# Kernel optimization log

Measured on AMD Instinct MI355X. Metric: run time of the kernel, lower is better.

## Reference

```python
import jax, jax.numpy as jnp
import numpy as np
import math

RATIOS = [2, 4, 8, 16]   # attn_aggr_ratio per path
HEAD_DIM = 64
EPS = 1e-5               # BatchNorm1d eps (eval mode, running stats)


def _bn(x, g, b, m, v):
    # x: (N, C, L); per-channel eval-mode BatchNorm1d
    inv = g / jnp.sqrt(v + EPS)
    return x * inv[None, :, None] + (b - m * inv)[None, :, None]


def _conv1(x, W, b=None):
    # 1x1 Conv1d == channel matmul. x: (N, Cin, L), W: (Cout, Cin)
    y = jnp.einsum('ncl,dc->ndl', x, W)
    if b is not None:
        y = y + b[None, :, None]
    return y


def setup_inputs() -> dict:
    key = jax.random.key(0)
    ks = iter(jax.random.split(key, 16))
    N, C, L = 8, 512, 3072
    P, d = 4, C // 4
    FF = 4 * C
    w = lambda shape: jax.random.normal(next(ks), shape, dtype=jnp.float32) * 0.05
    inp = {'x': jax.random.normal(next(ks), (N, C, L), dtype=jnp.float32)}
    for nm in ('norm1', 'norm2'):
        inp[nm + '_g'] = jnp.ones((C,), jnp.float32)
        inp[nm + '_b'] = jnp.zeros((C,), jnp.float32)
        inp[nm + '_m'] = jnp.zeros((C,), jnp.float32)
        inp[nm + '_v'] = jnp.ones((C,), jnp.float32)
    for nm in ('Wq', 'Wk', 'Wv', 'Wo', 'Wp'):
        inp[nm] = w((P, d, d))
    for nm in ('bq', 'bk', 'bv', 'bo'):
        inp[nm] = jnp.zeros((P, d), jnp.float32)
    for nm in ('ag', 'an'):  # aggr-block BN and pre-KV BN, per path
        inp[nm + '_g'] = jnp.ones((P, d), jnp.float32)
        inp[nm + '_b'] = jnp.zeros((P, d), jnp.float32)
        inp[nm + '_m'] = jnp.zeros((P, d), jnp.float32)
        inp[nm + '_v'] = jnp.ones((P, d), jnp.float32)
    inp['W1'] = w((FF, C)); inp['b1'] = jnp.zeros((FF,), jnp.float32)
    inp['W2'] = w((C, FF)); inp['b2'] = jnp.zeros((C,), jnp.float32)
    return inp


def reference(x, norm1_g, norm1_b, norm1_m, norm1_v,
              Wq, bq, Wk, bk, Wv, bv, Wo, bo, Wp,
              ag_g, ag_b, ag_m, ag_v, an_g, an_b, an_m, an_v,
              norm2_g, norm2_b, norm2_m, norm2_v,
              W1, b1, W2, b2):
    N, C, L = x.shape
    P = len(RATIOS)
    d = C // P
    h = _bn(x, norm1_g, norm1_b, norm1_m, norm1_v)
    outs = []
    for i, r in enumerate(RATIOS):  # small fixed set of paths
        xi = h[:, i * d:(i + 1) * d, :]                       # (N, d, L)
        q = _conv1(xi, Wq[i], bq[i])                          # (N, d, L)
        # local aware aggregation: avg_pool + max_pool (L divisible by r)
        xp = xi.reshape(N, d, L // r, r)
        xa = xp.mean(-1) + xp.max(-1)                         # (N, d, L/r)
        xa = _bn(_conv1(xa, Wp[i]), ag_g[i], ag_b[i], ag_m[i], ag_v[i])
        xa = _bn(xa, an_g[i], an_b[i], an_m[i], an_v[i])
        k = _conv1(xa, Wk[i], bk[i])
        v = _conv1(xa, Wv[i], bv[i])
        Nh = d // HEAD_DIM
        Lk = L // r
        qh = q.reshape(N, Nh, HEAD_DIM, L) / math.sqrt(HEAD_DIM)
        kh = k.reshape(N, Nh, HEAD_DIM, Lk)
        vh = v.reshape(N, Nh, HEAD_DIM, Lk)
        attn = jax.nn.softmax(jnp.einsum('nhel,nhem->nhlm', qh, kh), axis=-1)
        o = jnp.einsum('nhlm,nhem->nhel', attn, vh).reshape(N, d, L)
        outs.append(_conv1(o, Wo[i], bo[i]))
    x = x + jnp.concatenate(outs, axis=1)                     # residual
    h2 = _bn(x, norm2_g, norm2_b, norm2_m, norm2_v)
    m = jax.nn.gelu(_conv1(h2, W1, b1))
    m = _conv1(m, W2, b2)
    return x + m
```

## Files before the change

kernel.cpp:

```cpp
#include <hip/hip_runtime.h>
#include <math.h>

#define EPS 1e-5f

#define F_BIAS  1
#define F_DBN   2
#define F_GELU  4
#define F_RESID 8

typedef __attribute__((ext_vector_type(8))) __bf16 bf16x8;
typedef __attribute__((ext_vector_type(4))) float f32x4;
typedef __attribute__((ext_vector_type(8))) unsigned short u16x8;

__device__ __forceinline__ unsigned int pack2bf(float a, float b) {
    unsigned short ua = __builtin_bit_cast(unsigned short, (__bf16)a);
    unsigned short ub = __builtin_bit_cast(unsigned short, (__bf16)b);
    return (unsigned int)ua | ((unsigned int)ub << 16);
}

__device__ __forceinline__ void gload_lds16(const unsigned short* g, unsigned short* l) {
    __builtin_amdgcn_global_load_lds(
        (const __attribute__((address_space(1))) unsigned int*)g,
        (__attribute__((address_space(3))) unsigned int*)l,
        16, 0, 0);
}

__device__ __forceinline__ float gelu_f(float u) {
    float s = u * u;
    float w = u * fmaf(s, 0.0713548162726f, 1.59576912161f);
    float e = __expf(-w);
    return u * __builtin_amdgcn_rcpf(1.f + e);
}

__device__ __constant__ int c_LKS[4]  = {1536, 768, 384, 192};
__device__ __constant__ int c_OFFB[4] = {0, 1572864, 2359296, 2752512};

__global__ __launch_bounds__(256) void wcvt_kernel(
    const float* __restrict__ Wq, const float* __restrict__ Wk,
    const float* __restrict__ Wv, const float* __restrict__ Wo,
    const float* __restrict__ Wp, const float* __restrict__ W1,
    const float* __restrict__ W2, unsigned short* __restrict__ dst)
{
    const int WSZ = 65536;
    const int FSZ = 1048576;
    int i4 = blockIdx.x * blockDim.x + threadIdx.x;
    long long i = (long long)i4 * 4;
    const long long total = 5LL * WSZ + 2LL * FSZ;
    if (i >= total) return;
    #pragma unroll
    for (int j = 0; j < 4; ++j) {
        long long idx = i + j;
        float v;
        if      (idx < WSZ)            v = Wq[idx];
        else if (idx < 2 * WSZ)        v = Wk[idx - WSZ];
        else if (idx < 3 * WSZ)        v = Wv[idx - 2 * WSZ];
        else if (idx < 4 * WSZ)        v = Wo[idx - 3 * WSZ];
        else if (idx < 5 * WSZ)        v = Wp[idx - 4 * WSZ];
        else if (idx < 5 * WSZ + FSZ)  v = W1[idx - 5 * WSZ];
        else                           v = W2[idx - 5 * WSZ - FSZ];
        dst[idx] = __builtin_bit_cast(unsigned short, (__bf16)v);
    }
}

__global__ __launch_bounds__(256) void bn_transpose_kernel(
    const float* __restrict__ x,
    const float* __restrict__ g, const float* __restrict__ b,
    const float* __restrict__ bm, const float* __restrict__ bvv,
    unsigned short* __restrict__ hT, int C, int L)
{
    __shared__ float ps[64][65];
    const int l0 = blockIdx.x * 64, ct = blockIdx.y, n = blockIdx.z;
    const int tid = threadIdx.x;
    const int c = tid >> 2, q = tid & 3;
    const int cg = ct * 64 + c;
    float inv = g[cg] * rsqrtf(bvv[cg] + EPS);
    float add = b[cg] - bm[cg] * inv;
    const float* xp = x + ((size_t)n * C + cg) * L + l0 + q * 16;
    #pragma unroll
    for (int s = 0; s < 4; ++s) {
        float4 vv = *(const float4*)&xp[s * 4];
        ps[c][q * 16 + s * 4 + 0] = fmaf(vv.x, inv, add);
        ps[c][q * 16 + s * 4 + 1] = fmaf(vv.y, inv, add);
        ps[c][q * 16 + s * 4 + 2] = fmaf(vv.z, inv, add);
        ps[c][q * 16 + s * 4 + 3] = fmaf(vv.w, inv, add);
    }
    __syncthreads();
    #pragma unroll
    for (int j = 0; j < 2; ++j) {
        int row = (tid >> 3) + 32 * j;
        int cc0 = (tid & 7) * 8;
        unsigned int w0 = pack2bf(ps[cc0 + 0][row], ps[cc0 + 1][row]);
        unsigned int w1 = pack2bf(ps[cc0 + 2][row], ps[cc0 + 3][row]);
        unsigned int w2 = pack2bf(ps[cc0 + 4][row], ps[cc0 + 5][row]);
        unsigned int w3 = pack2bf(ps[cc0 + 6][row], ps[cc0 + 7][row]);
        *(uint4*)&hT[((size_t)n * L + l0 + row) * C + ct * 64 + cc0] =
            make_uint4(w0, w1, w2, w3);
    }
}

__global__ __launch_bounds__(256) void pool_bn_all_kernel(
    const float* __restrict__ x,
    const float* __restrict__ g, const float* __restrict__ b,
    const float* __restrict__ bm, const float* __restrict__ bvv,
    unsigned short* __restrict__ xa0T_all, int C, int L)
{
    const int p = blockIdx.z & 3;
    const int n = blockIdx.z >> 2;
    const int Lk = c_LKS[p];
    const int lk0 = blockIdx.x * 64;
    if (lk0 >= Lk) return;
    const int r = L / Lk;
    const int ct = blockIdx.y;
    __shared__ float ps[64][65];
    const int tid = threadIdx.x;
    const int c = tid >> 2, q = tid & 3;
    const int cg = p * 128 + ct * 64 + c;
    float inv = g[cg] * rsqrtf(bvv[cg] + EPS);
    float add = b[cg] - bm[cg] * inv;
    const float* xp = x + ((size_t)n * C + cg) * L;
    float rinv = 1.0f / (float)r;
    #pragma unroll
    for (int s = 0; s < 16; ++s) {
        int lk = q * 16 + s;
        const float* base = xp + (size_t)(lk0 + lk) * r;
        float sum = 0.f, mx = -INFINITY;
        for (int j = 0; j < r; j += 2) {
            float2 vv = *(const float2*)&base[j];
            float t0 = fmaf(vv.x, inv, add);
            float t1 = fmaf(vv.y, inv, add);
            sum += t0 + t1;
            mx = fmaxf(mx, fmaxf(t0, t1));
        }
        ps[c][lk] = sum * rinv + mx;
    }
    __syncthreads();
    unsigned short* dst = xa0T_all + c_OFFB[p];
    #pragma unroll
    for (int j = 0; j < 2; ++j) {
        int row = (tid >> 3) + 32 * j;
        int cc0 = (tid & 7) * 8;
        unsigned int w0 = pack2bf(ps[cc0 + 0][row], ps[cc0 + 1][row]);
        unsigned int w1 = pack2bf(ps[cc0 + 2][row], ps[cc0 + 3][row]);
        unsigned int w2 = pack2bf(ps[cc0 + 4][row], ps[cc0 + 5][row]);
        unsigned int w3 = pack2bf(ps[cc0 + 6][row], ps[cc0 + 7][row]);
        *(uint4*)&dst[((size_t)n * Lk + lk0 + row) * 128 + ct * 64 + cc0] =
            make_uint4(w0, w1, w2, w3);
    }
}

template<int OMODE>
__global__ __launch_bounds__(256) void gemm_bf(
    const unsigned short* __restrict__ A, const unsigned short* __restrict__ BT,
    int M, int K, int Npos, int ldBT, long long strideBT,
    const float* __restrict__ bias, float oscale, int flags,
    const float* __restrict__ g1, const float* __restrict__ b1p,
    const float* __restrict__ m1p, const float* __restrict__ v1p,
    const float* __restrict__ g2, const float* __restrict__ b2p,
    const float* __restrict__ m2p, const float* __restrict__ v2p,
    float* __restrict__ outN, long long strideN,
    const float* __restrict__ resid, long long strideR,
    unsigned short* __restrict__ outT, int ldT, int moff, long long strideT,
    int gKoff)
{
    __shared__ __align__(16) unsigned short As[2][128][32];
    __shared__ __align__(16) unsigned short Bs[2][128][32];

    const int tid = threadIdx.x;

    const int gdx = gridDim.x, gdy = gridDim.y;
    const int nwg = gdx * gdy * gridDim.z;
    int bid = blockIdx.x + gdx * (blockIdx.y + gdy * blockIdx.z);
    {
        int q = nwg >> 3, rr = nwg & 7;
        int xcd = bid & 7, idx = bid >> 3;
        bid = (xcd < rr ? xcd * (q + 1) : rr * (q + 1) + (xcd - rr) * q) + idx;
    }
    const int bx = bid % gdx;
    const int by = (bid / gdx) % gdy;
    const int bz = bid / (gdx * gdy);

    const int m0 = by * 128;
    const int p0 = bx * 128;
    const unsigned short* Bn = BT + (size_t)bz * strideBT
                              + (size_t)(m0 >> 7) * gKoff;

    const int wave = tid >> 6;
    const int lane = tid & 63;
    const int qcol = lane & 15;
    const int hi   = lane >> 4;
    const int wr   = wave >> 1;
    const int wc   = wave & 1;
    const int lrow = lane >> 2;
    const int lseg = (lane & 3) * 8;

    const unsigned short* aR0 = A + (size_t)(m0 + wave * 32 + lrow) * K + lseg;
    const unsigned short* aR1 = aR0 + (size_t)16 * K;
    int pr0 = p0 + wave * 32 + lrow;      if (pr0 > Npos - 1) pr0 = Npos - 1;
    int pr1 = p0 + wave * 32 + 16 + lrow; if (pr1 > Npos - 1) pr1 = Npos - 1;
    const unsigned short* bR0 = Bn + (size_t)pr0 * ldBT + lseg;
    const unsigned short* bR1 = Bn + (size_t)pr1 * ldBT + lseg;
    unsigned short* ldsA0 = &As[0][wave * 32][0];
    unsigned short* ldsA1 = &As[0][wave * 32 + 16][0];
    unsigned short* ldsB0 = &Bs[0][wave * 32][0];
    unsigned short* ldsB1 = &Bs[0][wave * 32 + 16][0];
    const int bufStride = 128 * 32;

    auto STAGE = [&](int b, int t) {
        const int ko = t * 32;
        gload_lds16(aR0 + ko, ldsA0 + b * bufStride);
        gload_lds16(aR1 + ko, ldsA1 + b * bufStride);
        gload_lds16(bR0 + ko, ldsB0 + b * bufStride);
        gload_lds16(bR1 + ko, ldsB1 + b * bufStride);
    };

    f32x4 acc[4][4] = {};
    const int nt = K >> 5;

    STAGE(0, 0);
    STAGE(1, 1);

    auto MFMA_STEP = [&](int b) {
        bf16x8 af[4], bfr[4];
        #pragma unroll
        for (int mi = 0; mi < 4; ++mi)
            af[mi] = *(const bf16x8*)&As[b][wr * 64 + mi * 16 + qcol][hi * 8];
        #pragma unroll
        for (int ni = 0; ni < 4; ++ni)
            bfr[ni] = *(const bf16x8*)&Bs[b][wc * 64 + ni * 16 + qcol][hi * 8];
        #pragma unroll
        for (int mi = 0; mi < 4; ++mi)
            #pragma unroll
            for (int ni = 0; ni < 4; ++ni)
                acc[mi][ni] = __builtin_amdgcn_mfma_f32_16x16x32_bf16(
                    af[mi], bfr[ni], acc[mi][ni], 0, 0, 0);
    };

    int cur = 0;
    for (int t = 0; t < nt - 1; ++t) {
        asm volatile("s_waitcnt vmcnt(4)" ::: "memory");
        __builtin_amdgcn_s_barrier();
        MFMA_STEP(cur);
        __builtin_amdgcn_s_barrier();
        if (t + 2 < nt) STAGE(cur, t + 2);
        cur ^= 1;
    }
    asm volatile("s_waitcnt vmcnt(0)" ::: "memory");
    __builtin_amdgcn_s_barrier();
    MFMA_STEP(cur);

    float* Cn = outN + (size_t)bz * strideN;
    const float* Rn = resid + (size_t)bz * strideR;
    unsigned short* Tn = outT + (size_t)bz * strideT;

    #pragma unroll
    for (int mi = 0; mi < 4; ++mi) {
        const int mb = m0 + wr * 64 + mi * 16 + hi * 4;
        float4 bv4 = make_float4(0.f, 0.f, 0.f, 0.f);
        if (flags & F_BIAS) bv4 = *(const float4*)&bias[mb];
        float s1[4], t1[4];
        if ((flags & F_DBN) || OMODE == 3) {
            float4 gg = *(const float4*)&g1[mb];
            float4 bb = *(const float4*)&b1p[mb];
            float4 mm = *(const float4*)&m1p[mb];
            float4 vv = *(const float4*)&v1p[mb];
            float gga[4] = {gg.x, gg.y, gg.z, gg.w};
            float bba[4] = {bb.x, bb.y, bb.z, bb.w};
            float mma[4] = {mm.x, mm.y, mm.z, mm.w};
            float vva[4] = {vv.x, vv.y, vv.z, vv.w};
            #pragma unroll
            for (int r2 = 0; r2 < 4; ++r2) {
                float iv = gga[r2] * rsqrtf(vva[r2] + EPS);
                s1[r2] = iv; t1[r2] = bba[r2] - mma[r2] * iv;
            }
        }
        float s2[4], t2[4];
        if (flags & F_DBN) {
            float4 gg = *(const float4*)&g2[mb];
            float4 bb = *(const float4*)&b2p[mb];
            float4 mm = *(const float4*)&m2p[mb];
            float4 vv = *(const float4*)&v2p[mb];
            float gga[4] = {gg.x, gg.y, gg.z, gg.w};
            float bba[4] = {bb.x, bb.y, bb.z, bb.w};
            float mma[4] = {mm.x, mm.y, mm.z, mm.w};
            float vva[4] = {vv.x, vv.y, vv.z, vv.w};
            #pragma unroll
            for (int r2 = 0; r2 < 4; ++r2) {
                float iv = gga[r2] * rsqrtf(vva[r2] + EPS);
                s2[r2] = iv; t2[r2] = bba[r2] - mma[r2] * iv;
            }
        }
        const float ba[4] = {bv4.x, bv4.y, bv4.z, bv4.w};
        #pragma unroll
        for (int ni = 0; ni < 4; ++ni) {
            const int cp = p0 + wc * 64 + ni * 16 + qcol;
            if (cp >= Npos) continue;
            float vals[4];
            #pragma unroll
            for (int r2 = 0; r2 < 4; ++r2) {
                float val = (acc[mi][ni][r2] + ba[r2]) * oscale;
                if (flags & F_DBN) {
                    val = fmaf(val, s1[r2], t1[r2]);
                    val = fmaf(val, s2[r2], t2[r2]);
                }
                if (flags & F_GELU) val = gelu_f(val);
                vals[r2] = val;
            }
            if (OMODE == 0 || OMODE == 3) {
                #pragma unroll
                for (int r2 = 0; r2 < 4; ++r2) {
                    size_t off = (size_t)(mb + r2) * Npos + cp;
                    float v = vals[r2];
                    if (flags & F_RESID) v += Rn[off];
                    Cn[off] = v;
                    vals[r2] = v;
                }
            }
            if (OMODE == 1) {
                *(uint2*)&Tn[(size_t)cp * ldT + moff + mb] =
                    make_uint2(pack2bf(vals[0], vals[1]), pack2bf(vals[2], vals[3]));
            }
            if (OMODE == 2) {
                #pragma unroll
                for (int r2 = 0; r2 < 4; ++r2)
                    Tn[(size_t)(mb + r2) * Npos + cp] =
                        __builtin_bit_cast(unsigned short, (__bf16)vals[r2]);
            }
            if (OMODE == 3) {
                float a0 = fmaf(vals[0], s1[0], t1[0]);
                float a1 = fmaf(vals[1], s1[1], t1[1]);
                float a2 = fmaf(vals[2], s1[2], t1[2]);
                float a3 = fmaf(vals[3], s1[3], t1[3]);
                *(uint2*)&Tn[(size_t)cp * ldT + moff + mb] =
                    make_uint2(pack2bf(a0, a1), pack2bf(a2, a3));
            }
        }
    }
}

template<int OMODE, int FLAGS>
__global__ __launch_bounds__(512, 1) void gemm_bf256(
    const unsigned short* __restrict__ A, const unsigned short* __restrict__ BT,
    int K, int Npos, int ldBT, long long strideBT,
    const float* __restrict__ bias,
    float* __restrict__ outN, long long strideN,
    const float* __restrict__ resid, long long strideR,
    unsigned short* __restrict__ outT, int ldT, long long strideT)
{
    __shared__ __align__(16) unsigned short As[2][256][64];
    __shared__ __align__(16) unsigned short Bs[2][256][64];

    const int tid = threadIdx.x;

    const int gdx = gridDim.x, gdy = gridDim.y;
    const int nwg = gdx * gdy * gridDim.z;
    int bid = blockIdx.x + gdx * (blockIdx.y + gdy * blockIdx.z);
    {
        int q = nwg >> 3, rr = nwg & 7;
        int xcd = bid & 7, idx = bid >> 3;
        bid = (xcd < rr ? xcd * (q + 1) : rr * (q + 1) + (xcd - rr) * q) + idx;
    }
    const int bx = bid % gdx;
    const int by = (bid / gdx) % gdy;
    const int bz = bid / (gdx * gdy);

    const int m0 = by * 256;
    const int p0 = bx * 256;
    const unsigned short* Bn = BT + (size_t)bz * strideBT;

    const int wave = tid >> 6;
    const int lane = tid & 63;
    const int qcol = lane & 15;
    const int hi   = lane >> 4;
    const int wr   = wave >> 2;
    const int wc   = wave & 3;

    const int srow = lane >> 3;
    const int sxor = ((lane & 7) ^ srow) * 8;

    const unsigned short* aS = A + (size_t)(m0 + wave * 32 + srow) * K + sxor;
    const unsigned short* bS = Bn + (size_t)(p0 + wave * 32 + srow) * ldBT + sxor;
    unsigned short* ldsA = &As[0][wave * 32][0];
    unsigned short* ldsB = &Bs[0][wave * 32][0];
    const int bufStride = 256 * 64;

    auto STAGE = [&](int b, int t) {
        const int ko = t * 64;
        #pragma unroll
        for (int j = 0; j < 4; ++j) {
            gload_lds16(aS + (size_t)(j * 8) * K + ko,
                        ldsA + b * bufStride + j * 8 * 64);
            gload_lds16(bS + (size_t)(j * 8) * ldBT + ko,
                        ldsB + b * bufStride + j * 8 * 64);
        }
    };

    const int xr0 = (hi ^ (qcol & 7)) * 8;

    f32x4 acc[8][4] = {};
    const int nt = K >> 6;

    STAGE(0, 0);
    STAGE(1, 1);

    auto MFMA_STEP = [&](int b) {
        #pragma unroll
        for (int kk = 0; kk < 2; ++kk) {
            const int xx = xr0 ^ (kk << 5);
            bf16x8 af[8], bfr[4];
            #pragma unroll
            for (int mi = 0; mi < 8; ++mi)
                af[mi] = *(const bf16x8*)&As[b][wr * 128 + mi * 16 + qcol][xx];
            #pragma unroll
            for (int ni = 0; ni < 4; ++ni)
                bfr[ni] = *(const bf16x8*)&Bs[b][wc * 64 + ni * 16 + qcol][xx];
            #pragma unroll
            for (int mi = 0; mi < 8; ++mi)
                #pragma unroll
                for (int ni = 0; ni < 4; ++ni)
                    acc[mi][ni] = __builtin_amdgcn_mfma_f32_16x16x32_bf16(
                        af[mi], bfr[ni], acc[mi][ni], 0, 0, 0);
        }
    };

    int cur = 0;
    for (int t = 0; t < nt - 1; ++t) {
        asm volatile("s_waitcnt vmcnt(8)" ::: "memory");
        __builtin_amdgcn_s_barrier();
        MFMA_STEP(cur);
        __builtin_amdgcn_s_barrier();
        if (t + 2 < nt) STAGE(cur, t + 2);
        cur ^= 1;
    }
    asm volatile("s_waitcnt vmcnt(0)" ::: "memory");
    __builtin_amdgcn_s_barrier();
    MFMA_STEP(cur);

    float* Cn = outN + (size_t)bz * strideN;
    const float* Rn = resid + (size_t)bz * strideR;
    unsigned short* Tn = outT + (size_t)bz * strideT;

    #pragma unroll
    for (int mi = 0; mi < 8; ++mi) {
        const int mb = m0 + wr * 128 + mi * 16 + hi * 4;
        float ba[4] = {0.f, 0.f, 0.f, 0.f};
        if (FLAGS & F_BIAS) {
            float4 bv4 = *(const float4*)&bias[mb];
            ba[0] = bv4.x; ba[1] = bv4.y; ba[2] = bv4.z; ba[3] = bv4.w;
        }
        #pragma unroll
        for (int ni = 0; ni < 4; ++ni) {
            const int cp = p0 + wc * 64 + ni * 16 + qcol;
            float vals[4];
            #pragma unroll
            for (int r2 = 0; r2 < 4; ++r2) {
                float val = acc[mi][ni][r2] + ba[r2];
                if (FLAGS & F_GELU) val = gelu_f(val);
                vals[r2] = val;
            }
            if (OMODE == 0) {
                #pragma unroll
                for (int r2 = 0; r2 < 4; ++r2) {
                    size_t off = (size_t)(mb + r2) * Npos + cp;
                    float v = vals[r2];
                    if (FLAGS & F_RESID) v += Rn[off];
                    Cn[off] = v;
                }
            } else {
                *(uint2*)&Tn[(size_t)cp * ldT + mb] =
                    make_uint2(pack2bf(vals[0], vals[1]), pack2bf(vals[2], vals[3]));
            }
        }
    }
}

template<int MODE>
__global__ __launch_bounds__(256) void gemm_path(
    const unsigned short* __restrict__ A0, const unsigned short* __restrict__ A1,
    const unsigned short* __restrict__ Bsrc,
    const float* __restrict__ bias0, const float* __restrict__ bias1,
    const float* __restrict__ agg, const float* __restrict__ agb,
    const float* __restrict__ agm, const float* __restrict__ agv,
    const float* __restrict__ ang, const float* __restrict__ anb,
    const float* __restrict__ anm, const float* __restrict__ anv,
    unsigned short* __restrict__ out0, unsigned short* __restrict__ out1)
{
    __shared__ __align__(16) unsigned short As[2][128][32];
    __shared__ __align__(16) unsigned short Bs[2][128][32];

    const int tid = threadIdx.x;
    const int gdx = gridDim.x, gdy = gridDim.y;
    const int nwg = gdx * gdy * gridDim.z;
    int bid = blockIdx.x + gdx * (blockIdx.y + gdy * blockIdx.z);
    {
        int q = nwg >> 3, rr = nwg & 7;
        int xcd = bid & 7, idx = bid >> 3;
        bid = (xcd < rr ? xcd * (q + 1) : rr * (q + 1) + (xcd - rr) * q) + idx;
    }
    const int bx = bid % gdx;
    const int by = (bid / gdx) % gdy;
    const int bz = bid / (gdx * gdy);

    int p, px;
    if      (bx < 12) { p = 0; px = bx; }
    else if (bx < 18) { p = 1; px = bx - 12; }
    else if (bx < 21) { p = 2; px = bx - 18; }
    else              { p = 3; px = bx - 21; }
    const int Lk = c_LKS[p];
    const int offb = c_OFFB[p];
    const int c0 = p * 128;
    const int p0 = px * 128;
    const int K = 128;

    const unsigned short* A = (MODE == 1 && by == 1 ? A1 : A0) + p * 16384;
    const unsigned short* Bn = Bsrc + offb + (size_t)bz * Lk * 128;

    const int wave = tid >> 6;
    const int lane = tid & 63;
    const int qcol = lane & 15;
    const int hi   = lane >> 4;
    const int wr   = wave >> 1;
    const int wc   = wave & 1;
    const int lrow = lane >> 2;
    const int lseg = (lane & 3) * 8;

    const unsigned short* aR0 = A + (size_t)(wave * 32 + lrow) * K + lseg;
    const unsigned short* aR1 = aR0 + (size_t)16 * K;
    int pr0 = p0 + wave * 32 + lrow;      if (pr0 > Lk - 1) pr0 = Lk - 1;
    int pr1 = p0 + wave * 32 + 16 + lrow; if (pr1 > Lk - 1) pr1 = Lk - 1;
    const unsigned short* bR0 = Bn + (size_t)pr0 * 128 + lseg;
    const unsigned short* bR1 = Bn + (size_t)pr1 * 128 + lseg;
    unsigned short* ldsA0 = &As[0][wave * 32][0];
    unsigned short* ldsA1 = &As[0][wave * 32 + 16][0];
    unsigned short* ldsB0 = &Bs[0][wave * 32][0];
    unsigned short* ldsB1 = &Bs[0][wave * 32 + 16][0];
    const int bufStride = 128 * 32;

    auto STAGE = [&](int b, int t) {
        const int ko = t * 32;
        gload_lds16(aR0 + ko, ldsA0 + b * bufStride);
        gload_lds16(aR1 + ko, ldsA1 + b * bufStride);
        gload_lds16(bR0 + ko, ldsB0 + b * bufStride);
        gload_lds16(bR1 + ko, ldsB1 + b * bufStride);
    };

    f32x4 acc[4][4] = {};
    STAGE(0, 0);
    STAGE(1, 1);

    auto MFMA_STEP = [&](int b) {
        bf16x8 af[4], bfr[4];
        #pragma unroll
        for (int mi = 0; mi < 4; ++mi)
            af[mi] = *(const bf16x8*)&As[b][wr * 64 + mi * 16 + qcol][hi * 8];
        #pragma unroll
        for (int ni = 0; ni < 4; ++ni)
            bfr[ni] = *(const bf16x8*)&Bs[b][wc * 64 + ni * 16 + qcol][hi * 8];
        #pragma unroll
        for (int mi = 0; mi < 4; ++mi)
            #pragma unroll
            for (int ni = 0; ni < 4; ++ni)
                acc[mi][ni] = __builtin_amdgcn_mfma_f32_16x16x32_bf16(
                    af[mi], bfr[ni], acc[mi][ni], 0, 0, 0);
    };

    int cur = 0;
    const int nt = 4;
    for (int t = 0; t < nt - 1; ++t) {
        asm volatile("s_waitcnt vmcnt(4)" ::: "memory");
        __builtin_amdgcn_s_barrier();
        MFMA_STEP(cur);
        __builtin_amdgcn_s_barrier();
        if (t + 2 < nt) STAGE(cur, t + 2);
        cur ^= 1;
    }
    asm volatile("s_waitcnt vmcnt(0)" ::: "memory");
    __builtin_amdgcn_s_barrier();
    MFMA_STEP(cur);

    const bool isV = (MODE == 1 && by == 1);
    unsigned short* Tn = (isV ? out1 : out0) + offb + (size_t)bz * Lk * 128;
    const float* bias = (MODE == 0) ? nullptr : (by == 0 ? bias0 : bias1);

    #pragma unroll
    for (int mi = 0; mi < 4; ++mi) {
        const int mb = wr * 64 + mi * 16 + hi * 4;
        float ba[4] = {0.f, 0.f, 0.f, 0.f};
        if (MODE == 1) {
            float4 bv4 = *(const float4*)&bias[c0 + mb];
            ba[0] = bv4.x; ba[1] = bv4.y; ba[2] = bv4.z; ba[3] = bv4.w;
        }
        float s1[4], t1[4], s2[4], t2[4];
        if (MODE == 0) {
            #pragma unroll
            for (int r2 = 0; r2 < 4; ++r2) {
                int gm = c0 + mb + r2;
                float i1 = agg[gm] * rsqrtf(agv[gm] + EPS);
                s1[r2] = i1; t1[r2] = agb[gm] - agm[gm] * i1;
                float i2 = ang[gm] * rsqrtf(anv[gm] + EPS);
                s2[r2] = i2; t2[r2] = anb[gm] - anm[gm] * i2;
            }
        }
        #pragma unroll
        for (int ni = 0; ni < 4; ++ni) {
            const int cp = p0 + wc * 64 + ni * 16 + qcol;
            if (cp >= Lk) continue;
            float vals[4];
            #pragma unroll
            for (int r2 = 0; r2 < 4; ++r2) {
                float val = acc[mi][ni][r2] + ba[r2];
                if (MODE == 0) {
                    val = fmaf(val, s1[r2], t1[r2]);
                    val = fmaf(val, s2[r2], t2[r2]);
                }
                vals[r2] = val;
            }
            if (!isV) {
                *(uint2*)&Tn[(size_t)cp * 128 + mb] =
                    make_uint2(pack2bf(vals[0], vals[1]), pack2bf(vals[2], vals[3]));
            } else {
                #pragma unroll
                for (int r2 = 0; r2 < 4; ++r2)
                    Tn[(size_t)(mb + r2) * Lk + cp] =
                        __builtin_bit_cast(unsigned short, (__bf16)vals[r2]);
            }
        }
    }
}

__global__ __launch_bounds__(256) void attn_bf_all_kernel(
    const unsigned short* __restrict__ qT, const unsigned short* __restrict__ kT_all,
    const unsigned short* __restrict__ vN_all, unsigned short* __restrict__ obT,
    int L)
{
    const int p = blockIdx.z;
    const int Lk = c_LKS[p];
    const int offb = c_OFFB[p];
    const int l0 = blockIdx.x * 64;
    const int nh = blockIdx.y;
    const int n = nh >> 1, h = nh & 1;
    const unsigned short* qn = qT + (size_t)n * L * 512 + p * 128 + h * 64;
    const unsigned short* kn = kT_all + offb + (size_t)n * Lk * 128 + h * 64;
    const unsigned short* vn = vN_all + offb + ((size_t)n * 128 + h * 64) * Lk;
    unsigned short*       on = obT + (size_t)n * L * 512 + p * 128 + h * 64;

    __shared__ __align__(16) unsigned short Ks[2][64][64];
    __shared__ __align__(16) unsigned short Vs[2][64][64];
    __shared__ __align__(16) unsigned short Ps[4][16][72];

    const int tid = threadIdx.x;
    const int wave = tid >> 6;
    const int lane = tid & 63;
    const int qcol = lane & 15;
    const int hi   = lane >> 4;
    const int ql   = wave * 16 + qcol;

    const int srow = lane >> 3;
    const int sxor = (lane & 7) ^ srow;
    const unsigned short* kS0 = kn + (size_t)(wave * 16 + srow) * 128 + sxor * 8;
    const unsigned short* kS1 = kn + (size_t)(wave * 16 + 8 + srow) * 128 + sxor * 8;
    const unsigned short* vS0 = vn + (size_t)(wave * 16 + srow) * Lk + sxor * 8;
    const unsigned short* vS1 = vn + (size_t)(wave * 16 + 8 + srow) * Lk + sxor * 8;
    unsigned short* ldsK0 = &Ks[0][wave * 16][0];
    unsigned short* ldsK1 = &Ks[0][wave * 16 + 8][0];
    unsigned short* ldsV0 = &Vs[0][wave * 16][0];
    unsigned short* ldsV1 = &Vs[0][wave * 16 + 8][0];
    const int bufStride = 64 * 64;

    auto STAGE = [&](int b, int t) {
        const int mc = t * 64;
        gload_lds16(kS0 + (size_t)mc * 128, ldsK0 + b * bufStride);
        gload_lds16(kS1 + (size_t)mc * 128, ldsK1 + b * bufStride);
        gload_lds16(vS0 + mc, ldsV0 + b * bufStride);
        gload_lds16(vS1 + mc, ldsV1 + b * bufStride);
    };

    const int x0 = (hi ^ (qcol & 7)) * 8;
    const int x1 = x0 ^ 32;

    bf16x8 qf0 = *(const bf16x8*)&qn[(size_t)(l0 + ql) * 512 + hi * 8];
    bf16x8 qf1 = *(const bf16x8*)&qn[(size_t)(l0 + ql) * 512 + 32 + hi * 8];

    f32x4 o_acc[4] = {};
    float mrow = -INFINITY, lrow = 0.f;
    const int nt = Lk >> 6;

    STAGE(0, 0);
    STAGE(1, 1);

    auto COMPUTE = [&](int b) {
        f32x4 sacc[4];
        #pragma unroll
        for (int kt = 0; kt < 4; ++kt) {
            bf16x8 k0 = *(const bf16x8*)&Ks[b][kt * 16 + qcol][x0];
            bf16x8 k1 = *(const bf16x8*)&Ks[b][kt * 16 + qcol][x1];
            f32x4 a = {};
            a = __builtin_amdgcn_mfma_f32_16x16x32_bf16(k0, qf0, a, 0, 0, 0);
            a = __builtin_amdgcn_mfma_f32_16x16x32_bf16(k1, qf1, a, 0, 0, 0);
            sacc[kt] = a;
        }
        float m0 = fmaxf(fmaxf(sacc[0][0], sacc[0][1]), fmaxf(sacc[0][2], sacc[0][3]));
        float m1 = fmaxf(fmaxf(sacc[1][0], sacc[1][1]), fmaxf(sacc[1][2], sacc[1][3]));
        float m2 = fmaxf(fmaxf(sacc[2][0], sacc[2][1]), fmaxf(sacc[2][2], sacc[2][3]));
        float m3 = fmaxf(fmaxf(sacc[3][0], sacc[3][1]), fmaxf(sacc[3][2], sacc[3][3]));
        float cm = fmaxf(fmaxf(m0, m1), fmaxf(m2, m3));
        cm = fmaxf(cm, __shfl_xor(cm, 16));
        cm = fmaxf(cm, __shfl_xor(cm, 32));
        float nm = fmaxf(mrow, cm);
        float alpha = __expf(mrow - nm);
        float csum = 0.f;
        unsigned int pw[4][2];
        #pragma unroll
        for (int kt = 0; kt < 4; ++kt) {
            float p0 = __expf(sacc[kt][0] - nm);
            float p1 = __expf(sacc[kt][1] - nm);
            float p2 = __expf(sacc[kt][2] - nm);
            float p3 = __expf(sacc[kt][3] - nm);
            csum += (p0 + p1) + (p2 + p3);
            pw[kt][0] = pack2bf(p0, p1);
            pw[kt][1] = pack2bf(p2, p3);
        }
        csum += __shfl_xor(csum, 16);
        csum += __shfl_xor(csum, 32);
        lrow = lrow * alpha + csum;
        mrow = nm;

        #pragma unroll
        for (int kt = 0; kt < 4; ++kt)
            *(uint2*)&Ps[wave][qcol][kt * 16 + hi * 4] =
                make_uint2(pw[kt][0], pw[kt][1]);

        #pragma unroll
        for (int et = 0; et < 4; ++et)
            #pragma unroll
            for (int r2 = 0; r2 < 4; ++r2) o_acc[et][r2] *= alpha;

        bf16x8 pf0 = *(const bf16x8*)&Ps[wave][qcol][hi * 8];
        bf16x8 pf1 = *(const bf16x8*)&Ps[wave][qcol][hi * 8 + 32];
        #pragma unroll
        for (int et = 0; et < 4; ++et) {
            bf16x8 v0 = *(const bf16x8*)&Vs[b][et * 16 + qcol][x0];
            bf16x8 v1 = *(const bf16x8*)&Vs[b][et * 16 + qcol][x1];
            o_acc[et] = __builtin_amdgcn_mfma_f32_16x16x32_bf16(v0, pf0, o_acc[et], 0, 0, 0);
            o_acc[et] = __builtin_amdgcn_mfma_f32_16x16x32_bf16(v1, pf1, o_acc[et], 0, 0, 0);
        }
    };

    int cur = 0;
    for (int t = 0; t < nt - 1; ++t) {
        asm volatile("s_waitcnt vmcnt(4)" ::: "memory");
        __builtin_amdgcn_s_barrier();
        COMPUTE(cur);
        __builtin_amdgcn_s_barrier();
        if (t + 2 < nt) STAGE(cur, t + 2);
        cur ^= 1;
    }
    asm volatile("s_waitcnt vmcnt(0)" ::: "memory");
    __builtin_amdgcn_s_barrier();
    COMPUTE(cur);

    float invl = 1.f / lrow;
    #pragma unroll
    for (int et = 0; et < 4; ++et) {
        float a0 = o_acc[et][0] * invl, a1 = o_acc[et][1] * invl;
        float a2 = o_acc[et][2] * invl, a3 = o_acc[et][3] * invl;
        *(uint2*)&on[(size_t)(l0 + ql) * 512 + et * 16 + hi * 4] =
            make_uint2(pack2bf(a0, a1), pack2bf(a2, a3));
    }
}

extern "C" void kernel_launch(void* const* d_in, const int* in_sizes, int n_in,
                              void* d_out, int out_size, void* d_ws, size_t ws_size,
                              hipStream_t stream)
{
    const float* x   = (const float*)d_in[0];
    const float* n1g = (const float*)d_in[1];
    const float* n1b = (const float*)d_in[2];
    const float* n1m = (const float*)d_in[3];
    const float* n1v = (const float*)d_in[4];
    const float* n2g = (const float*)d_in[5];
    const float* n2b = (const float*)d_in[6];
    const float* n2m = (const float*)d_in[7];
    const float* n2v = (const float*)d_in[8];
    const float* Wq  = (const float*)d_in[9];
    const float* Wk  = (const float*)d_in[10];
    const float* Wv  = (const float*)d_in[11];
    const float* Wo  = (const float*)d_in[12];
    const float* Wp  = (const float*)d_in[13];
    const float* bq  = (const float*)d_in[14];
    const float* bk  = (const float*)d_in[15];
    const float* bv  = (const float*)d_in[16];
    const float* bo  = (const float*)d_in[17];
    const float* agg = (const float*)d_in[18];
    const float* agb = (const float*)d_in[19];
    const float* agm = (const float*)d_in[20];
    const float* agv = (const float*)d_in[21];
    const float* ang = (const float*)d_in[22];
    const float* anb = (const float*)d_in[23];
    const float* anm = (const float*)d_in[24];
    const float* anv = (const float*)d_in[25];
    const float* W1  = (const float*)d_in[26];
    const float* b1  = (const float*)d_in[27];
    const float* W2  = (const float*)d_in[28];
    const float* b2  = (const float*)d_in[29];

    float* out = (float*)d_out;
    unsigned short* wsb = (unsigned short*)d_ws;

    const int N = 8, Cc = 512, L = 3072, FF = 2048;
    const int WSZ = 65536, FSZ = 1048576;
    const size_t PATHBUF = 2949120;

    unsigned short* wbf      = wsb;
    unsigned short* hT       = wbf      + 5 * WSZ + 2 * FSZ;
    unsigned short* h2T      = hT;
    unsigned short* obT      = hT       + (size_t)N * L * Cc;
    unsigned short* xa0T_all = obT      + (size_t)N * L * 512;
    unsigned short* xabT_all = xa0T_all + PATHBUF;
    unsigned short* kT_all   = xabT_all + PATHBUF;
    unsigned short* vN_all   = kT_all   + PATHBUF;
    unsigned short* m1T      = vN_all   + PATHBUF;
    unsigned short* qTall    = m1T;

    const unsigned short* WqB = wbf;
    const unsigned short* WkB = wbf + WSZ;
    const unsigned short* WvB = wbf + 2 * WSZ;
    const unsigned short* WoB = wbf + 3 * WSZ;
    const unsigned short* WpB = wbf + 4 * WSZ;
    const unsigned short* W1B = wbf + 5 * WSZ;
    const unsigned short* W2B = wbf + 5 * WSZ + FSZ;

    const float* nul = nullptr;
    float* nulf = nullptr;
    unsigned short* nulu = nullptr;

    {
        long long tot4 = (5LL * WSZ + 2LL * FSZ) / 4;
        wcvt_kernel<<<dim3((unsigned)((tot4 + 255) / 256)), dim3(256), 0, stream>>>(
            Wq, Wk, Wv, Wo, Wp, W1, W2, wbf);
    }
    bn_transpose_kernel<<<dim3(L / 64, Cc / 64, N), dim3(256), 0, stream>>>(
        x, n1g, n1b, n1m, n1v, hT, Cc, L);

    pool_bn_all_kernel<<<dim3(24, 2, N * 4), dim3(256), 0, stream>>>(
        x, n1g, n1b, n1m, n1v, xa0T_all, Cc, L);

    gemm_bf<1><<<dim3(L / 128, 4, N), dim3(256), 0, stream>>>(
        WqB, hT, 512, 128, L, Cc, (long long)L * Cc,
        bq, 0.125f, F_BIAS,
        nul, nul, nul, nul, nul, nul, nul, nul,
        nulf, 0, nul, 0, qTall, 512, 0, (long long)L * 512, 128);

    gemm_path<0><<<dim3(23, 1, N), dim3(256), 0, stream>>>(
        WpB, nulu, xa0T_all, nul, nul,
        agg, agb, agm, agv, ang, anb, anm, anv,
        xabT_all, nulu);

    gemm_path<1><<<dim3(23, 2, N), dim3(256), 0, stream>>>(
        WkB, WvB, xabT_all, bk, bv,
        nul, nul, nul, nul, nul, nul, nul, nul,
        kT_all, vN_all);

    attn_bf_all_kernel<<<dim3(L / 64, N * 2, 4), dim3(256), 0, stream>>>(
        qTall, kT_all, vN_all, obT, L);

    gemm_bf<3><<<dim3(L / 128, 4, N), dim3(256), 0, stream>>>(
        WoB, obT, 512, 128, L, 512, (long long)L * 512,
        bo, 1.f, F_BIAS | F_RESID,
        n2g, n2b, n2m, n2v,
        nul, nul, nul, nul,
        out, (long long)Cc * L,
        x, (long long)Cc * L,
        h2T, Cc, 0, (long long)L * Cc, 128);

    gemm_bf256<1, F_BIAS | F_GELU><<<dim3(L / 256, FF / 256, N), dim3(512), 0, stream>>>(
        W1B, h2T, Cc, L, Cc, (long long)L * Cc,
        b1,
        nulf, 0, nul, 0,
        m1T, FF, (long long)L * FF);

    gemm_bf256<0, F_BIAS | F_RESID><<<dim3(L / 256, Cc / 256, N), dim3(512), 0, stream>>>(
        W2B, m1T, FF, L, FF, (long long)L * FF,
        b2,
        out, (long long)Cc * L, out, (long long)Cc * L,
        nulu, 0, 0);
}
```

Before: 517.1 us.

## Split GEMM K-loop into four quadrant phases with interleaved async LDS staging

Measured after the change: 507.9 us. About the same (-1.8%).

```diff
diff --git a/kernel.cpp b/kernel.cpp
--- a/kernel.cpp
+++ b/kernel.cpp
@@ -374,24 +374,47 @@
     const int wr   = wave >> 2;
     const int wc   = wave & 3;
 
-    const int srow = lane >> 3;
-    const int sxor = ((lane & 7) ^ srow) * 8;
-
-    const unsigned short* aS = A + (size_t)(m0 + wave * 32 + srow) * K + sxor;
-    const unsigned short* bS = Bn + (size_t)(p0 + wave * 32 + srow) * ldBT + sxor;
-    unsigned short* ldsA = &As[0][wave * 32][0];
-    unsigned short* ldsB = &Bs[0][wave * 32][0];
-    const int bufStride = 256 * 64;
-
-    auto STAGE = [&](int b, int t) {
-        const int ko = t * 64;
-        #pragma unroll
-        for (int j = 0; j < 4; ++j) {
-            gload_lds16(aS + (size_t)(j * 8) * K + ko,
-                        ldsA + b * bufStride + j * 8 * 64);
-            gload_lds16(bS + (size_t)(j * 8) * ldBT + ko,
-                        ldsB + b * bufStride + j * 8 * 64);
-        }
+    const int lrow8 = lane >> 3;
+    const int scol  = ((lane & 7) ^ lrow8) * 8;
+
+    const int rb0 = wave * 16, rb1 = rb0 + 8;
+    const int pa00 = rb0 + ((rb0 >> 6) << 6);
+    const int pa01 = rb1 + ((rb1 >> 6) << 6);
+    const int pa10 = 64 + rb0 + ((rb0 >> 6) << 6);
+    const int pa11 = 64 + rb1 + ((rb1 >> 6) << 6);
+    const int pb00 = ((rb0 >> 5) << 6) + (rb0 & 31);
+    const int pb01 = ((rb1 >> 5) << 6) + (rb1 & 31);
+    const int pb10 = ((rb0 >> 5) << 6) + 32 + (rb0 & 31);
+    const int pb11 = ((rb1 >> 5) << 6) + 32 + (rb1 & 31);
+
+    const unsigned short* sa00 = A + (size_t)(m0 + pa00 + lrow8) * K + scol;
+    const unsigned short* sa01 = A + (size_t)(m0 + pa01 + lrow8) * K + scol;
+    const unsigned short* sa10 = A + (size_t)(m0 + pa10 + lrow8) * K + scol;
+    const unsigned short* sa11 = A + (size_t)(m0 + pa11 + lrow8) * K + scol;
+    const unsigned short* sb00 = Bn + (size_t)(p0 + pb00 + lrow8) * ldBT + scol;
+    const unsigned short* sb01 = Bn + (size_t)(p0 + pb01 + lrow8) * ldBT + scol;
+    const unsigned short* sb10 = Bn + (size_t)(p0 + pb10 + lrow8) * ldBT + scol;
+    const unsigned short* sb11 = Bn + (size_t)(p0 + pb11 + lrow8) * ldBT + scol;
+
+    auto STAGE_A0 = [&](int buf, int tt) {
+        const int ko = tt * 64;
+        gload_lds16(sa00 + ko, &As[buf][pa00][0]);
+        gload_lds16(sa01 + ko, &As[buf][pa01][0]);
+    };
+    auto STAGE_A1 = [&](int buf, int tt) {
+        const int ko = tt * 64;
+        gload_lds16(sa10 + ko, &As[buf][pa10][0]);
+        gload_lds16(sa11 + ko, &As[buf][pa11][0]);
+    };
+    auto STAGE_B0 = [&](int buf, int tt) {
+        const int ko = tt * 64;
+        gload_lds16(sb00 + ko, &Bs[buf][pb00][0]);
+        gload_lds16(sb01 + ko, &Bs[buf][pb01][0]);
+    };
+    auto STAGE_B1 = [&](int buf, int tt) {
+        const int ko = tt * 64;
+        gload_lds16(sb10 + ko, &Bs[buf][pb10][0]);
+        gload_lds16(sb11 + ko, &Bs[buf][pb11][0]);
     };
 
     const int xr0 = (hi ^ (qcol & 7)) * 8;
@@ -399,41 +422,63 @@
     f32x4 acc[8][4] = {};
     const int nt = K >> 6;
 
-    STAGE(0, 0);
-    STAGE(1, 1);
-
-    auto MFMA_STEP = [&](int b) {
-        #pragma unroll
-        for (int kk = 0; kk < 2; ++kk) {
-            const int xx = xr0 ^ (kk << 5);
-            bf16x8 af[8], bfr[4];
-            #pragma unroll
-            for (int mi = 0; mi < 8; ++mi)
-                af[mi] = *(const bf16x8*)&As[b][wr * 128 + mi * 16 + qcol][xx];
-            #pragma unroll
-            for (int ni = 0; ni < 4; ++ni)
-                bfr[ni] = *(const bf16x8*)&Bs[b][wc * 64 + ni * 16 + qcol][xx];
-            #pragma unroll
-            for (int mi = 0; mi < 8; ++mi)
-                #pragma unroll
-                for (int ni = 0; ni < 4; ++ni)
-                    acc[mi][ni] = __builtin_amdgcn_mfma_f32_16x16x32_bf16(
-                        af[mi], bfr[ni], acc[mi][ni], 0, 0, 0);
-        }
-    };
+    STAGE_A0(0, 0); STAGE_B0(0, 0); STAGE_A1(0, 0); STAGE_B1(0, 0);
+    if (nt > 1) { STAGE_A0(1, 1); STAGE_B0(1, 1); }
+    asm volatile("s_waitcnt vmcnt(4)" ::: "memory");
+    __builtin_amdgcn_s_barrier();
+
+#define PH_READ(a, b)                                                         \
+    bf16x8 af[4][2], bfr[2][2];                                               \
+    _Pragma("unroll") for (int m2 = 0; m2 < 4; ++m2)                          \
+    _Pragma("unroll") for (int kk = 0; kk < 2; ++kk)                          \
+        af[m2][kk] = *(const bf16x8*)&As[cur][wr * 128 + (a) * 64 + m2 * 16 + qcol][xr0 ^ (kk << 5)]; \
+    _Pragma("unroll") for (int n2 = 0; n2 < 2; ++n2)                          \
+    _Pragma("unroll") for (int kk = 0; kk < 2; ++kk)                          \
+        bfr[n2][kk] = *(const bf16x8*)&Bs[cur][wc * 64 + ((b) * 2 + n2) * 16 + qcol][xr0 ^ (kk << 5)];
+
+#define PH_MMA(a, b)                                                          \
+    __builtin_amdgcn_s_barrier();                                             \
+    __builtin_amdgcn_s_setprio(1);                                            \
+    _Pragma("unroll") for (int m2 = 0; m2 < 4; ++m2)                          \
+    _Pragma("unroll") for (int n2 = 0; n2 < 2; ++n2)                          \
+    _Pragma("unroll") for (int kk = 0; kk < 2; ++kk)                          \
+        acc[(a) * 4 + m2][(b) * 2 + n2] = __builtin_amdgcn_mfma_f32_16x16x32_bf16( \
+            af[m2][kk], bfr[n2][kk], acc[(a) * 4 + m2][(b) * 2 + n2], 0, 0, 0);    \
+    __builtin_amdgcn_s_setprio(0);                                            \
+    __builtin_amdgcn_s_barrier();
 
     int cur = 0;
-    for (int t = 0; t < nt - 1; ++t) {
-        asm volatile("s_waitcnt vmcnt(8)" ::: "memory");
-        __builtin_amdgcn_s_barrier();
-        MFMA_STEP(cur);
-        __builtin_amdgcn_s_barrier();
-        if (t + 2 < nt) STAGE(cur, t + 2);
-        cur ^= 1;
-    }
-    asm volatile("s_waitcnt vmcnt(0)" ::: "memory");
-    __builtin_amdgcn_s_barrier();
-    MFMA_STEP(cur);
+    for (int t = 0; t < nt; ++t) {
+        const int nxt = cur ^ 1;
+        {
+            PH_READ(0, 0)
+            if (t + 1 < nt) STAGE_A1(nxt, t + 1);
+            PH_MMA(0, 0)
+        }
+        {
+            PH_READ(0, 1)
+            if (t + 1 < nt) STAGE_B1(nxt, t + 1);
+            PH_MMA(0, 1)
+        }
+        {
+            PH_READ(1, 0)
+            if (t + 2 < nt) STAGE_A0(cur, t + 2);
+            PH_MMA(1, 0)
+        }
+        {
+            PH_READ(1, 1)
+            if (t + 2 < nt) STAGE_B0(cur, t + 2);
+            if (t + 2 < nt) {
+                asm volatile("s_waitcnt vmcnt(4)" ::: "memory");
+            } else if (t + 2 == nt) {
+                asm volatile("s_waitcnt vmcnt(0)" ::: "memory");
+            }
+            PH_MMA(1, 1)
+        }
+        cur = nxt;
+    }
+#undef PH_READ
+#undef PH_MMA
 
     float* Cn = outN + (size_t)bz * strideN;
     const float* Rn = resid + (size_t)bz * strideR;
```

## Switch GEMM to 4-stage K=32 LDS pipeline with MFMA priority boost

Applied to the files above, without the earlier changes.

Measured after the change: 533.1 us. 3.1% more time.

```diff
diff --git a/kernel.cpp b/kernel.cpp
--- a/kernel.cpp
+++ b/kernel.cpp
@@ -346,8 +346,8 @@
     const float* __restrict__ resid, long long strideR,
     unsigned short* __restrict__ outT, int ldT, long long strideT)
 {
-    __shared__ __align__(16) unsigned short As[2][256][64];
-    __shared__ __align__(16) unsigned short Bs[2][256][64];
+    __shared__ __align__(16) unsigned short As[4][256][32];
+    __shared__ __align__(16) unsigned short Bs[4][256][32];
 
     const int tid = threadIdx.x;
 
@@ -374,66 +374,62 @@
     const int wr   = wave >> 2;
     const int wc   = wave & 3;
 
-    const int srow = lane >> 3;
-    const int sxor = ((lane & 7) ^ srow) * 8;
-
-    const unsigned short* aS = A + (size_t)(m0 + wave * 32 + srow) * K + sxor;
-    const unsigned short* bS = Bn + (size_t)(p0 + wave * 32 + srow) * ldBT + sxor;
-    unsigned short* ldsA = &As[0][wave * 32][0];
-    unsigned short* ldsB = &Bs[0][wave * 32][0];
-    const int bufStride = 256 * 64;
+    const int lrow4 = lane >> 2;
+    const int sseg  = ((lane & 3) ^ (lrow4 & 3)) * 8;
+
+    const unsigned short* aS0 = A + (size_t)(m0 + wave * 32 + lrow4) * K + sseg;
+    const unsigned short* aS1 = aS0 + (size_t)16 * K;
+    const unsigned short* bS0 = Bn + (size_t)(p0 + wave * 32 + lrow4) * ldBT + sseg;
+    const unsigned short* bS1 = bS0 + (size_t)16 * ldBT;
+    unsigned short* ldsA0 = &As[0][wave * 32][0];
+    unsigned short* ldsA1 = &As[0][wave * 32 + 16][0];
+    unsigned short* ldsB0 = &Bs[0][wave * 32][0];
+    unsigned short* ldsB1 = &Bs[0][wave * 32 + 16][0];
+    const int bufStride = 256 * 32;
 
     auto STAGE = [&](int b, int t) {
-        const int ko = t * 64;
-        #pragma unroll
-        for (int j = 0; j < 4; ++j) {
-            gload_lds16(aS + (size_t)(j * 8) * K + ko,
-                        ldsA + b * bufStride + j * 8 * 64);
-            gload_lds16(bS + (size_t)(j * 8) * ldBT + ko,
-                        ldsB + b * bufStride + j * 8 * 64);
-        }
+        const int ko = t * 32;
+        gload_lds16(aS0 + ko, ldsA0 + b * bufStride);
+        gload_lds16(aS1 + ko, ldsA1 + b * bufStride);
+        gload_lds16(bS0 + ko, ldsB0 + b * bufStride);
+        gload_lds16(bS1 + ko, ldsB1 + b * bufStride);
     };
 
-    const int xr0 = (hi ^ (qcol & 7)) * 8;
+    const int xr = (hi ^ (qcol & 3)) * 8;
 
     f32x4 acc[8][4] = {};
-    const int nt = K >> 6;
-
-    STAGE(0, 0);
-    STAGE(1, 1);
+    const int nt = K >> 5;
+
+    STAGE(0, 0); STAGE(1, 1); STAGE(2, 2);
 
     auto MFMA_STEP = [&](int b) {
-        #pragma unroll
-        for (int kk = 0; kk < 2; ++kk) {
-            const int xx = xr0 ^ (kk << 5);
-            bf16x8 af[8], bfr[4];
-            #pragma unroll
-            for (int mi = 0; mi < 8; ++mi)
-                af[mi] = *(const bf16x8*)&As[b][wr * 128 + mi * 16 + qcol][xx];
+        bf16x8 af[8], bfr[4];
+        #pragma unroll
+        for (int mi = 0; mi < 8; ++mi)
+            af[mi] = *(const bf16x8*)&As[b][wr * 128 + mi * 16 + qcol][xr];
+        #pragma unroll
+        for (int ni = 0; ni < 4; ++ni)
+            bfr[ni] = *(const bf16x8*)&Bs[b][wc * 64 + ni * 16 + qcol][xr];
+        #pragma unroll
+        for (int mi = 0; mi < 8; ++mi)
             #pragma unroll
             for (int ni = 0; ni < 4; ++ni)
-                bfr[ni] = *(const bf16x8*)&Bs[b][wc * 64 + ni * 16 + qcol][xx];
-            #pragma unroll
-            for (int mi = 0; mi < 8; ++mi)
-                #pragma unroll
-                for (int ni = 0; ni < 4; ++ni)
-                    acc[mi][ni] = __builtin_amdgcn_mfma_f32_16x16x32_bf16(
-                        af[mi], bfr[ni], acc[mi][ni], 0, 0, 0);
-        }
+                acc[mi][ni] = __builtin_amdgcn_mfma_f32_16x16x32_bf16(
+                    af[mi], bfr[ni], acc[mi][ni], 0, 0, 0);
     };
 
-    int cur = 0;
-    for (int t = 0; t < nt - 1; ++t) {
-        asm volatile("s_waitcnt vmcnt(8)" ::: "memory");
+    for (int t = 0; t < nt; ++t) {
+        const int rem = nt - t;
+        if (rem >= 3)      { asm volatile("s_waitcnt vmcnt(8)" ::: "memory"); }
+        else if (rem == 2) { asm volatile("s_waitcnt vmcnt(4)" ::: "memory"); }
+        else               { asm volatile("s_waitcnt vmcnt(0)" ::: "memory"); }
         __builtin_amdgcn_s_barrier();
-        MFMA_STEP(cur);
+        __builtin_amdgcn_s_setprio(1);
+        MFMA_STEP(t & 3);
+        __builtin_amdgcn_s_setprio(0);
         __builtin_amdgcn_s_barrier();
-        if (t + 2 < nt) STAGE(cur, t + 2);
-        cur ^= 1;
-    }
-    asm volatile("s_waitcnt vmcnt(0)" ::: "memory");
-    __builtin_amdgcn_s_barrier();
-    MFMA_STEP(cur);
+        if (t + 3 < nt) STAGE((t + 3) & 3, t + 3);
+    }
 
     float* Cn = outN + (size_t)bz * strideN;
     const float* Rn = resid + (size_t)bz * strideR;
```
